# Optimization experiments

Measured on AMD Instinct MI355X. Metric: run time of the kernel, lower is better.

## Reference

```python
import jax, jax.numpy as jnp
import numpy as np
from jax.scipy.stats import norm

N_TOK = 4096
D_MODEL = 1024
D_FF = 2048
N_EXP = 8
K = 2
NOISE_EPS = 0.01          # noise_epsilon in noisy_top_k_gating
LOSS_COEF = 0.1
ZERO_FILL = float(np.finfo(float).eps)  # combined[combined == 0] = eps


def setup_inputs() -> dict:
    key = jax.random.key(0)
    ks = jax.random.split(key, 8)
    s = 0.02
    return {
        "x": jax.random.normal(ks[0], (N_TOK, D_MODEL), jnp.float32),
        "noise": jax.random.normal(ks[1], (N_TOK, N_EXP), jnp.float32),  # torch.randn_like(clean_logits)
        "w_gate": jax.random.normal(ks[2], (D_MODEL, N_EXP), jnp.float32) * s,
        "w_noise": jax.random.normal(ks[3], (D_MODEL, N_EXP), jnp.float32) * s,
        "w1": jax.random.normal(ks[4], (N_EXP, D_MODEL, D_FF), jnp.float32) * s,
        "b1": jnp.zeros((N_EXP, D_FF), jnp.float32),
        "w2": jax.random.normal(ks[5], (N_EXP, D_FF, D_MODEL), jnp.float32) * s,
        "b2": jnp.zeros((N_EXP, D_MODEL), jnp.float32),
    }


def _cv_squared(v):
    # torch .var() is unbiased (ddof=1)
    return jnp.var(v, ddof=1) / (jnp.mean(v) ** 2 + 1e-10)


def reference(x, noise, w_gate, w_noise, w1, b1, w2, b2):
    B = x.shape[0]
    # --- noisy top-k gating (train=True) ---
    clean_logits = x @ w_gate                                   # [B, E]
    noise_stddev = jax.nn.softplus(x @ w_noise) + NOISE_EPS     # [B, E]
    noisy_logits = clean_logits + noise * noise_stddev
    m = min(K + 1, N_EXP)
    top_vals, top_idx = jax.lax.top_k(noisy_logits, m)          # [B, k+1]
    top_k_gates = jax.nn.softmax(top_vals[:, :K], axis=1)       # [B, k]
    gates = jnp.zeros((B, N_EXP), x.dtype).at[
        jnp.arange(B)[:, None], top_idx[:, :K]
    ].set(top_k_gates)                                          # [B, E] sparse-in-values

    # --- load via _prob_in_top_k ---
    thr_in = top_vals[:, K][:, None]       # (k+1)-th noisy value
    thr_out = top_vals[:, K - 1][:, None]  # k-th noisy value
    is_in = noisy_logits > thr_in
    prob_if_in = norm.cdf((clean_logits - thr_in) / noise_stddev)
    prob_if_out = norm.cdf((clean_logits - thr_out) / noise_stddev)
    load = jnp.where(is_in, prob_if_in, prob_if_out).sum(0)     # [E]

    importance = gates.sum(0)
    loss = (_cv_squared(importance) + _cv_squared(load)) * LOSS_COEF

    # --- expert FFNs + gate-weighted combine ---
    # Dense-over-experts evaluation; gates are zero for non-selected experts,
    # so this is mathematically identical to dispatch/combine.
    h = jax.nn.relu(jnp.einsum('td,edf->tef', x, w1) + b1)      # [T, E, d_ff]
    expert_out = jnp.einsum('tef,efd->ted', h, w2) + b2         # [T, E, d_model]
    y = jnp.einsum('ted,te->td', expert_out, gates)             # [T, d_model]
    y = jnp.where(y == 0, ZERO_FILL, y)                         # combined[combined==0] = eps
    return y, loss
```

## Files before the change

### kernel.cpp

```cpp
#include <hip/hip_runtime.h>
#include <hip/hip_bf16.h>

#define N_TOK 4096
#define D_MODEL 1024
#define D_FF 2048
#define N_EXP 8

typedef __attribute__((ext_vector_type(8))) short short8;
typedef __attribute__((ext_vector_type(4))) float f32x4;

#define OFF_COUNTS 0
#define OFF_SEL    128
#define OFF_G0     16512
#define OFF_TOK    32896
#define OFF_GATE   295040
#define OFF_LOADV  426112
#define OFF_XB     1048576
#define OFF_W1T    9437184
#define OFF_W2T    42991616
#define OFF_H      76546048

__device__ __forceinline__ unsigned short f2bf(float f) {
  union { float f; unsigned u; } a; a.f = f;
  return (unsigned short)((a.u + 0x7FFFu + ((a.u >> 16) & 1u)) >> 16);
}

__device__ __forceinline__ void async16(const void* g, void* l) {
  __builtin_amdgcn_global_load_lds(
      (const __attribute__((address_space(1))) unsigned int*)g,
      (__attribute__((address_space(3))) unsigned int*)l, 16, 0, 0);
}

__global__ __launch_bounds__(256) void transpose_both_kernel(
    const float* __restrict__ w1, unsigned short* __restrict__ w1t,
    const float* __restrict__ w2, unsigned short* __restrict__ w2t) {
  const int bx = blockIdx.x;
  const float* in; unsigned short* out;
  int K, N, kb, nb, e;
  if (bx < 4096) {
    K = D_MODEL; N = D_FF;
    e = bx >> 9; const int rem = bx & 511;
    nb = (rem & 31) * 64; kb = (rem >> 5) * 64;
    in = w1; out = w1t;
  } else {
    K = D_FF; N = D_MODEL;
    const int b2x = bx - 4096;
    e = b2x >> 9; const int rem = b2x & 511;
    nb = (rem & 15) * 64; kb = (rem >> 4) * 64;
    in = w2; out = w2t;
  }
  __shared__ float tile[64][65];
  const int tid = threadIdx.x;
  const float* ine = in + (size_t)e * K * N;
  unsigned short* oute = out + (size_t)e * K * N;
  {
    const int c4 = tid & 15, rr = tid >> 4;
#pragma unroll
    for (int i = 0; i < 4; ++i) {
      const int row = i * 16 + rr;
      const float4 v = *(const float4*)(ine + (size_t)(kb + row) * N + nb + c4 * 4);
      tile[row][c4 * 4 + 0] = v.x;
      tile[row][c4 * 4 + 1] = v.y;
      tile[row][c4 * 4 + 2] = v.z;
      tile[row][c4 * 4 + 3] = v.w;
    }
  }
  __syncthreads();
  {
    const int n = tid >> 2, seg = tid & 3;
    unsigned short v[16];
#pragma unroll
    for (int j = 0; j < 16; ++j) v[j] = f2bf(tile[seg * 16 + j][n]);
    uint4* dst = (uint4*)(oute + (size_t)(nb + n) * K + kb + seg * 16);
    dst[0] = *(uint4*)&v[0];
    dst[1] = *(uint4*)&v[8];
  }
}

__global__ __launch_bounds__(256) void gating_kernel(
    const float* __restrict__ x, const float* __restrict__ noise,
    const float* __restrict__ wg, const float* __restrict__ wn,
    int* __restrict__ sel, float* __restrict__ g0out,
    float* __restrict__ loadvec, unsigned short* __restrict__ xb,
    int* __restrict__ counts) {
  if (blockIdx.x == 0 && threadIdx.x < N_EXP) counts[threadIdx.x] = 0;
  const int wave = threadIdx.x >> 6, lane = threadIdx.x & 63;
  const int t = blockIdx.x * 4 + wave;
  float ag[8], an[8];
#pragma unroll
  for (int e = 0; e < 8; ++e) { ag[e] = 0.f; an[e] = 0.f; }
  const float* xrow = x + (size_t)t * D_MODEL;
  for (int d = lane; d < D_MODEL; d += 64) {
    const float xv = xrow[d];
    const float4 wa = ((const float4*)(wg + (size_t)d * 8))[0];
    const float4 wb = ((const float4*)(wg + (size_t)d * 8))[1];
    const float4 na = ((const float4*)(wn + (size_t)d * 8))[0];
    const float4 nb = ((const float4*)(wn + (size_t)d * 8))[1];
    ag[0] += xv * wa.x; ag[1] += xv * wa.y; ag[2] += xv * wa.z; ag[3] += xv * wa.w;
    ag[4] += xv * wb.x; ag[5] += xv * wb.y; ag[6] += xv * wb.z; ag[7] += xv * wb.w;
    an[0] += xv * na.x; an[1] += xv * na.y; an[2] += xv * na.z; an[3] += xv * na.w;
    an[4] += xv * nb.x; an[5] += xv * nb.y; an[6] += xv * nb.z; an[7] += xv * nb.w;
  }
  {
    const float4* xv4 = (const float4*)xrow;
    ushort4* xb4 = (ushort4*)(xb + (size_t)t * D_MODEL);
#pragma unroll
    for (int i = 0; i < 4; ++i) {
      const float4 v = xv4[lane + i * 64];
      ushort4 o;
      o.x = f2bf(v.x); o.y = f2bf(v.y); o.z = f2bf(v.z); o.w = f2bf(v.w);
      xb4[lane + i * 64] = o;
    }
  }
#pragma unroll
  for (int e = 0; e < 8; ++e) {
#pragma unroll
    for (int off = 32; off > 0; off >>= 1) {
      ag[e] += __shfl_xor(ag[e], off, 64);
      an[e] += __shfl_xor(an[e], off, 64);
    }
  }
  float clean[8], sd[8], nz[8];
#pragma unroll
  for (int e = 0; e < 8; ++e) {
    clean[e] = ag[e];
    float s = an[e];
    s = (s > 20.f) ? s : log1pf(expf(s));
    sd[e] = s + 0.01f;
    nz[e] = clean[e] + noise[t * 8 + e] * sd[e];
  }
  float v0 = -1e30f, v1 = -1e30f, v2 = -1e30f; int i0 = 0, i1 = 0;
#pragma unroll
  for (int e = 0; e < 8; ++e) {
    const float v = nz[e];
    if (v > v0)      { v2 = v1; v1 = v0; i1 = i0; v0 = v; i0 = e; }
    else if (v > v1) { v2 = v1; v1 = v; i1 = e; }
    else if (v > v2) { v2 = v; }
  }
  const float ex = expf(v1 - v0);
  const float g0 = 1.f / (1.f + ex);
  if (lane == 0) { sel[t] = i0 | (i1 << 8); g0out[t] = g0; }
  if (lane < 8) {
    const int e = lane;
    const bool is_in = nz[e] > v2;
    const float thr = is_in ? v2 : v1;
    const float z = (clean[e] - thr) / sd[e];
    loadvec[t * 8 + e] = 0.5f * erfcf(-z * 0.70710678118654752f);
  }
}

__global__ __launch_bounds__(256) void build_lists_kernel(
    const int* __restrict__ sel, const float* __restrict__ g0a,
    int* __restrict__ counts, int* __restrict__ tok_list,
    float* __restrict__ gate_list) {
  __shared__ int hist[8], bbase[8];
  if (threadIdx.x < 8) hist[threadIdx.x] = 0;
  __syncthreads();
  const int t = blockIdx.x * 256 + threadIdx.x;
  const int s = sel[t];
  const int e0 = s & 255, e1 = (s >> 8) & 255;
  atomicAdd(&hist[e0], 1);
  atomicAdd(&hist[e1], 1);
  __syncthreads();
  if (threadIdx.x < 8) {
    bbase[threadIdx.x] = atomicAdd(&counts[threadIdx.x], hist[threadIdx.x]);
    hist[threadIdx.x] = 0;
  }
  __syncthreads();
  const float g = g0a[t];
  const int p0 = atomicAdd(&hist[e0], 1);
  const int idx0 = e0 * N_TOK + bbase[e0] + p0;
  tok_list[idx0] = t; gate_list[idx0] = g;
  const int p1 = atomicAdd(&hist[e1], 1);
  const int idx1 = e1 * N_TOK + bbase[e1] + p1;
  tok_list[idx1] = t; gate_list[idx1] = 1.f - g;
}

__global__ __launch_bounds__(256) void gemm1_kernel(
    const unsigned short* __restrict__ xb, const unsigned short* __restrict__ w1t,
    const float* __restrict__ b1,
    const int* __restrict__ counts,
    const int* __restrict__ tok_list, unsigned short* __restrict__ h) {
  const int e = blockIdx.x, nt = blockIdx.y, mt = blockIdx.z;
  const int cnt = counts[e];
  const int m0 = mt * 128;
  if (m0 >= cnt) return;
  int bs = 0;
#pragma unroll
  for (int i = 0; i < 8; ++i) bs += (i < e) ? counts[i] : 0;
  const int n0 = nt * 128;

  __shared__ __align__(16) unsigned short As[128 * 64];
  __shared__ __align__(16) unsigned short Bs[128 * 64];

  const int tid = threadIdx.x;
  const int wave = tid >> 6, lane = tid & 63;
  const int lrow = lane >> 3;
  const int scg  = (lane & 7) ^ lrow;

  const unsigned short* ap[4];
  const unsigned short* bp[4];
  unsigned short* adst[4];
  unsigned short* bdst[4];
#pragma unroll
  for (int c = 0; c < 4; ++c) {
    const int rr = wave * 32 + c * 8;
    const int arow = min(m0 + rr + lrow, cnt - 1);
    const int tok = tok_list[e * N_TOK + arow];
    ap[c] = xb + (size_t)tok * D_MODEL + scg * 8;
    bp[c] = w1t + (size_t)e * D_MODEL * D_FF + (size_t)(n0 + rr + lrow) * D_MODEL + scg * 8;
    adst[c] = As + rr * 64;
    bdst[c] = Bs + rr * 64;
  }

  const int wm = wave & 1, wn = wave >> 1;
  const int q = lane >> 4, r = lane & 15;
  const int r7 = r & 7;

  f32x4 acc[4][4];
#pragma unroll
  for (int a = 0; a < 4; ++a)
#pragma unroll
    for (int b = 0; b < 4; ++b) acc[a][b] = (f32x4){0.f, 0.f, 0.f, 0.f};

  for (int k0 = 0; k0 < D_MODEL; k0 += 64) {
#pragma unroll
    for (int c = 0; c < 4; ++c) {
      async16(ap[c], adst[c]);
      async16(bp[c], bdst[c]);
      ap[c] += 64; bp[c] += 64;
    }
    __syncthreads();
#pragma unroll
    for (int kk = 0; kk < 64; kk += 32) {
      const int gsw = (((kk >> 3) + q) ^ r7) * 8;
      short8 af[4], bfg[4];
#pragma unroll
      for (int t = 0; t < 4; ++t)
        af[t] = *(const short8*)(As + (wm * 64 + t * 16 + r) * 64 + gsw);
#pragma unroll
      for (int t = 0; t < 4; ++t)
        bfg[t] = *(const short8*)(Bs + (wn * 64 + t * 16 + r) * 64 + gsw);
#pragma unroll
      for (int tm = 0; tm < 4; ++tm)
#pragma unroll
        for (int tn = 0; tn < 4; ++tn)
          acc[tm][tn] = __builtin_amdgcn_mfma_f32_16x16x32_bf16(af[tm], bfg[tn], acc[tm][tn], 0, 0, 0);
    }
    __syncthreads();
  }

  float bv[4];
#pragma unroll
  for (int tn = 0; tn < 4; ++tn) bv[tn] = b1[e * D_FF + n0 + wn * 64 + tn * 16 + r];
#pragma unroll
  for (int tm = 0; tm < 4; ++tm) {
#pragma unroll
    for (int v = 0; v < 4; ++v) {
      const int i = wm * 64 + tm * 16 + q * 4 + v;
      if (m0 + i < cnt) {
        unsigned short* hrow = h + (size_t)(bs + m0 + i) * D_FF + n0 + wn * 64 + r;
#pragma unroll
        for (int tn = 0; tn < 4; ++tn)
          hrow[tn * 16] = f2bf(fmaxf(acc[tm][tn][v] + bv[tn], 0.f));
      }
    }
  }
}

__global__ __launch_bounds__(256) void gemm2_kernel(
    const unsigned short* __restrict__ h, const unsigned short* __restrict__ w2t,
    const float* __restrict__ b2,
    const int* __restrict__ counts,
    const int* __restrict__ tok_list, const float* __restrict__ gate_list,
    float* __restrict__ y) {
  const int e = blockIdx.x, nt = blockIdx.y;
  const int mt = blockIdx.z >> 1, kh = blockIdx.z & 1;
  const int cnt = counts[e];
  const int m0 = mt * 128;
  if (m0 >= cnt) return;
  int bs = 0;
#pragma unroll
  for (int i = 0; i < 8; ++i) bs += (i < e) ? counts[i] : 0;
  const int n0 = nt * 128;
  const int kbase = kh * (D_FF / 2);

  __shared__ __align__(16) unsigned short As[128 * 64];
  __shared__ __align__(16) unsigned short Bs[128 * 64];

  const int tid = threadIdx.x;
  const int wave = tid >> 6, lane = tid & 63;
  const int lrow = lane >> 3;
  const int scg  = (lane & 7) ^ lrow;

  const unsigned short* ap[4];
  const unsigned short* bp[4];
  unsigned short* adst[4];
  unsigned short* bdst[4];
#pragma unroll
  for (int c = 0; c < 4; ++c) {
    const int rr = wave * 32 + c * 8;
    const int arow = min(m0 + rr + lrow, cnt - 1);
    ap[c] = h + (size_t)(bs + arow) * D_FF + kbase + scg * 8;
    bp[c] = w2t + (size_t)e * D_MODEL * D_FF + (size_t)(n0 + rr + lrow) * D_FF + kbase + scg * 8;
    adst[c] = As + rr * 64;
    bdst[c] = Bs + rr * 64;
  }

  const int wm = wave & 1, wn = wave >> 1;
  const int q = lane >> 4, r = lane & 15;
  const int r7 = r & 7;

  f32x4 acc[4][4];
#pragma unroll
  for (int a = 0; a < 4; ++a)
#pragma unroll
    for (int b = 0; b < 4; ++b) acc[a][b] = (f32x4){0.f, 0.f, 0.f, 0.f};

  for (int k0 = 0; k0 < D_FF / 2; k0 += 64) {
#pragma unroll
    for (int c = 0; c < 4; ++c) {
      async16(ap[c], adst[c]);
      async16(bp[c], bdst[c]);
      ap[c] += 64; bp[c] += 64;
    }
    __syncthreads();
#pragma unroll
    for (int kk = 0; kk < 64; kk += 32) {
      const int gsw = (((kk >> 3) + q) ^ r7) * 8;
      short8 af[4], bfg[4];
#pragma unroll
      for (int t = 0; t < 4; ++t)
        af[t] = *(const short8*)(As + (wm * 64 + t * 16 + r) * 64 + gsw);
#pragma unroll
      for (int t = 0; t < 4; ++t)
        bfg[t] = *(const short8*)(Bs + (wn * 64 + t * 16 + r) * 64 + gsw);
#pragma unroll
      for (int tm = 0; tm < 4; ++tm)
#pragma unroll
        for (int tn = 0; tn < 4; ++tn)
          acc[tm][tn] = __builtin_amdgcn_mfma_f32_16x16x32_bf16(af[tm], bfg[tn], acc[tm][tn], 0, 0, 0);
    }
    __syncthreads();
  }

  float bv[4];
#pragma unroll
  for (int tn = 0; tn < 4; ++tn)
    bv[tn] = (kh == 0) ? b2[e * D_MODEL + n0 + wn * 64 + tn * 16 + r] : 0.f;
#pragma unroll
  for (int tm = 0; tm < 4; ++tm) {
#pragma unroll
    for (int v = 0; v < 4; ++v) {
      const int i = wm * 64 + tm * 16 + q * 4 + v;
      const int mrow = m0 + i;
      if (mrow < cnt) {
        const int idx = e * N_TOK + mrow;
        const int tok = tok_list[idx];
        const float g = gate_list[idx];
        float* orow = y + (size_t)tok * D_MODEL + n0 + wn * 64 + r;
#pragma unroll
        for (int tn = 0; tn < 4; ++tn)
          atomicAdd(&orow[tn * 16], (acc[tm][tn][v] + bv[tn]) * g);
      }
    }
  }
}

__global__ __launch_bounds__(256) void fixup_loss_kernel(
    float* __restrict__ y,
    const int* __restrict__ sel, const float* __restrict__ g0a,
    const float* __restrict__ loadvec) {
  const int i = blockIdx.x * 256 + threadIdx.x;
  float4 o = ((const float4*)y)[i];
  const float eps = 2.2204460492503131e-16f;
  if (o.x == 0.f) o.x = eps;
  if (o.y == 0.f) o.y = eps;
  if (o.z == 0.f) o.z = eps;
  if (o.w == 0.f) o.w = eps;
  ((float4*)y)[i] = o;

  if (blockIdx.x == 0) {
    float limp[8], lld[8];
#pragma unroll
    for (int e = 0; e < 8; ++e) { limp[e] = 0.f; lld[e] = 0.f; }
    for (int t = threadIdx.x; t < N_TOK; t += 256) {
      const int s = sel[t];
      const float g = g0a[t];
      const int e0 = s & 255, e1 = (s >> 8) & 255;
#pragma unroll
      for (int e = 0; e < 8; ++e)
        limp[e] += (e0 == e ? g : 0.f) + (e1 == e ? (1.f - g) : 0.f);
#pragma unroll
      for (int e = 0; e < 8; ++e) lld[e] += loadvec[t * 8 + e];
    }
#pragma unroll
    for (int e = 0; e < 8; ++e) {
#pragma unroll
      for (int off = 32; off > 0; off >>= 1) {
        limp[e] += __shfl_xor(limp[e], off, 64);
        lld[e]  += __shfl_xor(lld[e],  off, 64);
      }
    }
    __shared__ float red[4][16];
    const int wave = threadIdx.x >> 6, lane = threadIdx.x & 63;
    if (lane == 0) {
#pragma unroll
      for (int e = 0; e < 8; ++e) { red[wave][e] = limp[e]; red[wave][8 + e] = lld[e]; }
    }
    __syncthreads();
    if (threadIdx.x == 0) {
      double imp[8], ld[8];
      for (int e = 0; e < 8; ++e) {
        imp[e] = (double)red[0][e] + red[1][e] + red[2][e] + red[3][e];
        ld[e]  = (double)red[0][8 + e] + red[1][8 + e] + red[2][8 + e] + red[3][8 + e];
      }
      double mi = 0, ml = 0;
      for (int e = 0; e < 8; ++e) { mi += imp[e]; ml += ld[e]; }
      mi /= 8.0; ml /= 8.0;
      double vi = 0, vl = 0;
      for (int e = 0; e < 8; ++e) { vi += (imp[e] - mi) * (imp[e] - mi); vl += (ld[e] - ml) * (ld[e] - ml); }
      vi /= 7.0; vl /= 7.0;
      y[(size_t)N_TOK * D_MODEL] =
          (float)(0.1 * (vi / (mi * mi + 1e-10) + vl / (ml * ml + 1e-10)));
    }
  }
}

extern "C" void kernel_launch(void* const* d_in, const int* in_sizes, int n_in,
                              void* d_out, int out_size, void* d_ws, size_t ws_size,
                              hipStream_t stream) {
  const float* x     = (const float*)d_in[0];
  const float* noise = (const float*)d_in[1];
  const float* wg    = (const float*)d_in[2];
  const float* wn    = (const float*)d_in[3];
  const float* w1    = (const float*)d_in[4];
  const float* b1    = (const float*)d_in[5];
  const float* w2    = (const float*)d_in[6];
  const float* b2    = (const float*)d_in[7];
  float* out = (float*)d_out;

  char* ws = (char*)d_ws;
  int*   counts    = (int*)(ws + OFF_COUNTS);
  int*   sel       = (int*)(ws + OFF_SEL);
  float* g0a       = (float*)(ws + OFF_G0);
  int*   tok_list  = (int*)(ws + OFF_TOK);
  float* gate_list = (float*)(ws + OFF_GATE);
  float* loadvec   = (float*)(ws + OFF_LOADV);
  unsigned short* xb  = (unsigned short*)(ws + OFF_XB);
  unsigned short* w1t = (unsigned short*)(ws + OFF_W1T);
  unsigned short* w2t = (unsigned short*)(ws + OFF_W2T);
  unsigned short* h   = (unsigned short*)(ws + OFF_H);

  hipMemsetAsync(out, 0, (size_t)N_TOK * D_MODEL * sizeof(float), stream);

  gating_kernel<<<N_TOK / 4, 256, 0, stream>>>(x, noise, wg, wn, sel, g0a, loadvec, xb, counts);
  transpose_both_kernel<<<8192, 256, 0, stream>>>(w1, w1t, w2, w2t);
  build_lists_kernel<<<N_TOK / 256, 256, 0, stream>>>(sel, g0a, counts, tok_list, gate_list);
  gemm1_kernel<<<dim3(N_EXP, D_FF / 128, N_TOK / 128), 256, 0, stream>>>(
      xb, w1t, b1, counts, tok_list, h);
  gemm2_kernel<<<dim3(N_EXP, D_MODEL / 128, (N_TOK / 128) * 2), 256, 0, stream>>>(
      h, w2t, b2, counts, tok_list, gate_list, out);
  fixup_loss_kernel<<<(N_TOK * D_MODEL / 4) / 256, 256, 0, stream>>>(out, sel, g0a, loadvec);
}
```

Before: 383.3 us.

## Fuse MoE pipeline into one cooperative persistent kernel with split-output buffers

Merges the gating, weight transpose, list building, both expert GEMMs and the final fixup into a single cooperative persistent kernel, with grid.sync between phases. The second GEMM stops using atomicAdd into a zeroed output and instead writes into per-slot, per-K-half staging buffers that a final pass sums, so the output memset is gone as well. This removes several launches and the atomic contention, but adds grid-wide barriers, limits occupancy to what a cooperative launch allows, and adds extra staging traffic. The sout1 buffer reuses the w1t region after GEMM1 has finished with it.

```diff
diff --git a/kernel.cpp b/kernel.cpp
--- a/kernel.cpp
+++ b/kernel.cpp
@@ -1,5 +1,8 @@
 #include <hip/hip_runtime.h>
 #include <hip/hip_bf16.h>
+#include <hip/hip_cooperative_groups.h>
+
+namespace cg = cooperative_groups;
 
 #define N_TOK 4096
 #define D_MODEL 1024
@@ -19,6 +22,7 @@
 #define OFF_W1T    9437184
 #define OFF_W2T    42991616
 #define OFF_H      76546048
+#define OFF_SOUT   110100480
 
 __device__ __forceinline__ unsigned short f2bf(float f) {
   union { float f; unsigned u; } a; a.f = f;
@@ -31,398 +35,403 @@
       (__attribute__((address_space(3))) unsigned int*)l, 16, 0, 0);
 }
 
-__global__ __launch_bounds__(256) void transpose_both_kernel(
-    const float* __restrict__ w1, unsigned short* __restrict__ w1t,
-    const float* __restrict__ w2, unsigned short* __restrict__ w2t) {
-  const int bx = blockIdx.x;
-  const float* in; unsigned short* out;
-  int K, N, kb, nb, e;
-  if (bx < 4096) {
-    K = D_MODEL; N = D_FF;
-    e = bx >> 9; const int rem = bx & 511;
-    nb = (rem & 31) * 64; kb = (rem >> 5) * 64;
-    in = w1; out = w1t;
-  } else {
-    K = D_FF; N = D_MODEL;
-    const int b2x = bx - 4096;
-    e = b2x >> 9; const int rem = b2x & 511;
-    nb = (rem & 15) * 64; kb = (rem >> 4) * 64;
-    in = w2; out = w2t;
-  }
-  __shared__ float tile[64][65];
-  const int tid = threadIdx.x;
-  const float* ine = in + (size_t)e * K * N;
-  unsigned short* oute = out + (size_t)e * K * N;
-  {
-    const int c4 = tid & 15, rr = tid >> 4;
-#pragma unroll
-    for (int i = 0; i < 4; ++i) {
-      const int row = i * 16 + rr;
-      const float4 v = *(const float4*)(ine + (size_t)(kb + row) * N + nb + c4 * 4);
-      tile[row][c4 * 4 + 0] = v.x;
-      tile[row][c4 * 4 + 1] = v.y;
-      tile[row][c4 * 4 + 2] = v.z;
-      tile[row][c4 * 4 + 3] = v.w;
-    }
-  }
-  __syncthreads();
-  {
-    const int n = tid >> 2, seg = tid & 3;
-    unsigned short v[16];
-#pragma unroll
-    for (int j = 0; j < 16; ++j) v[j] = f2bf(tile[seg * 16 + j][n]);
-    uint4* dst = (uint4*)(oute + (size_t)(nb + n) * K + kb + seg * 16);
-    dst[0] = *(uint4*)&v[0];
-    dst[1] = *(uint4*)&v[8];
-  }
-}
-
-__global__ __launch_bounds__(256) void gating_kernel(
+__global__ __launch_bounds__(256, 3) void moe_mega_kernel(
     const float* __restrict__ x, const float* __restrict__ noise,
     const float* __restrict__ wg, const float* __restrict__ wn,
-    int* __restrict__ sel, float* __restrict__ g0out,
+    const float* __restrict__ w1, const float* __restrict__ b1,
+    const float* __restrict__ w2, const float* __restrict__ b2,
+    float* __restrict__ y,
+    int* __restrict__ sel, float* __restrict__ g0a,
+    int* __restrict__ tok_list, float* __restrict__ gate_list,
     float* __restrict__ loadvec, unsigned short* __restrict__ xb,
+    unsigned short* __restrict__ w1t, unsigned short* __restrict__ w2t,
+    unsigned short* __restrict__ h,
+    float* __restrict__ sout0, float* __restrict__ sout1,
     int* __restrict__ counts) {
-  if (blockIdx.x == 0 && threadIdx.x < N_EXP) counts[threadIdx.x] = 0;
-  const int wave = threadIdx.x >> 6, lane = threadIdx.x & 63;
-  const int t = blockIdx.x * 4 + wave;
-  float ag[8], an[8];
-#pragma unroll
-  for (int e = 0; e < 8; ++e) { ag[e] = 0.f; an[e] = 0.f; }
-  const float* xrow = x + (size_t)t * D_MODEL;
-  for (int d = lane; d < D_MODEL; d += 64) {
-    const float xv = xrow[d];
-    const float4 wa = ((const float4*)(wg + (size_t)d * 8))[0];
-    const float4 wb = ((const float4*)(wg + (size_t)d * 8))[1];
-    const float4 na = ((const float4*)(wn + (size_t)d * 8))[0];
-    const float4 nb = ((const float4*)(wn + (size_t)d * 8))[1];
-    ag[0] += xv * wa.x; ag[1] += xv * wa.y; ag[2] += xv * wa.z; ag[3] += xv * wa.w;
-    ag[4] += xv * wb.x; ag[5] += xv * wb.y; ag[6] += xv * wb.z; ag[7] += xv * wb.w;
-    an[0] += xv * na.x; an[1] += xv * na.y; an[2] += xv * na.z; an[3] += xv * na.w;
-    an[4] += xv * nb.x; an[5] += xv * nb.y; an[6] += xv * nb.z; an[7] += xv * nb.w;
+  __shared__ __align__(16) unsigned char smem[32768];
+  cg::grid_group grid = cg::this_grid();
+  const int b = blockIdx.x, tid = threadIdx.x;
+  const int nblk = gridDim.x;
+  const int wave = tid >> 6, lane = tid & 63;
+
+  if (b == 0 && tid < N_EXP) counts[tid] = 0;
+#pragma unroll 1
+  for (int t = b * 4 + wave; t < N_TOK; t += nblk * 4) {
+    float ag[8], an[8];
+#pragma unroll
+    for (int e = 0; e < 8; ++e) { ag[e] = 0.f; an[e] = 0.f; }
+    const float* xrow = x + (size_t)t * D_MODEL;
+    for (int d = lane; d < D_MODEL; d += 64) {
+      const float xv = xrow[d];
+      const float4 wa = ((const float4*)(wg + (size_t)d * 8))[0];
+      const float4 wb = ((const float4*)(wg + (size_t)d * 8))[1];
+      const float4 na = ((const float4*)(wn + (size_t)d * 8))[0];
+      const float4 nb = ((const float4*)(wn + (size_t)d * 8))[1];
+      ag[0] += xv * wa.x; ag[1] += xv * wa.y; ag[2] += xv * wa.z; ag[3] += xv * wa.w;
+      ag[4] += xv * wb.x; ag[5] += xv * wb.y; ag[6] += xv * wb.z; ag[7] += xv * wb.w;
+      an[0] += xv * na.x; an[1] += xv * na.y; an[2] += xv * na.z; an[3] += xv * na.w;
+      an[4] += xv * nb.x; an[5] += xv * nb.y; an[6] += xv * nb.z; an[7] += xv * nb.w;
+    }
+    {
+      const float4* xv4 = (const float4*)xrow;
+      ushort4* xb4 = (ushort4*)(xb + (size_t)t * D_MODEL);
+#pragma unroll
+      for (int i = 0; i < 4; ++i) {
+        const float4 v = xv4[lane + i * 64];
+        ushort4 o;
+        o.x = f2bf(v.x); o.y = f2bf(v.y); o.z = f2bf(v.z); o.w = f2bf(v.w);
+        xb4[lane + i * 64] = o;
+      }
+    }
+#pragma unroll
+    for (int e = 0; e < 8; ++e) {
+#pragma unroll
+      for (int off = 32; off > 0; off >>= 1) {
+        ag[e] += __shfl_xor(ag[e], off, 64);
+        an[e] += __shfl_xor(an[e], off, 64);
+      }
+    }
+    float clean[8], sd[8], nz[8];
+#pragma unroll
+    for (int e = 0; e < 8; ++e) {
+      clean[e] = ag[e];
+      float s = an[e];
+      s = (s > 20.f) ? s : log1pf(expf(s));
+      sd[e] = s + 0.01f;
+      nz[e] = clean[e] + noise[t * 8 + e] * sd[e];
+    }
+    float v0 = -1e30f, v1 = -1e30f, v2 = -1e30f; int i0 = 0, i1 = 0;
+#pragma unroll
+    for (int e = 0; e < 8; ++e) {
+      const float v = nz[e];
+      if (v > v0)      { v2 = v1; v1 = v0; i1 = i0; v0 = v; i0 = e; }
+      else if (v > v1) { v2 = v1; v1 = v; i1 = e; }
+      else if (v > v2) { v2 = v; }
+    }
+    const float ex = expf(v1 - v0);
+    const float g0 = 1.f / (1.f + ex);
+    if (lane == 0) { sel[t] = i0 | (i1 << 8); g0a[t] = g0; }
+    if (lane < 8) {
+      const int e = lane;
+      const bool is_in = nz[e] > v2;
+      const float thr = is_in ? v2 : v1;
+      const float z = (clean[e] - thr) / sd[e];
+      loadvec[t * 8 + e] = 0.5f * erfcf(-z * 0.70710678118654752f);
+    }
   }
   {
-    const float4* xv4 = (const float4*)xrow;
-    ushort4* xb4 = (ushort4*)(xb + (size_t)t * D_MODEL);
-#pragma unroll
-    for (int i = 0; i < 4; ++i) {
-      const float4 v = xv4[lane + i * 64];
-      ushort4 o;
-      o.x = f2bf(v.x); o.y = f2bf(v.y); o.z = f2bf(v.z); o.w = f2bf(v.w);
-      xb4[lane + i * 64] = o;
-    }
-  }
-#pragma unroll
-  for (int e = 0; e < 8; ++e) {
-#pragma unroll
-    for (int off = 32; off > 0; off >>= 1) {
-      ag[e] += __shfl_xor(ag[e], off, 64);
-      an[e] += __shfl_xor(an[e], off, 64);
-    }
-  }
-  float clean[8], sd[8], nz[8];
-#pragma unroll
-  for (int e = 0; e < 8; ++e) {
-    clean[e] = ag[e];
-    float s = an[e];
-    s = (s > 20.f) ? s : log1pf(expf(s));
-    sd[e] = s + 0.01f;
-    nz[e] = clean[e] + noise[t * 8 + e] * sd[e];
-  }
-  float v0 = -1e30f, v1 = -1e30f, v2 = -1e30f; int i0 = 0, i1 = 0;
-#pragma unroll
-  for (int e = 0; e < 8; ++e) {
-    const float v = nz[e];
-    if (v > v0)      { v2 = v1; v1 = v0; i1 = i0; v0 = v; i0 = e; }
-    else if (v > v1) { v2 = v1; v1 = v; i1 = e; }
-    else if (v > v2) { v2 = v; }
-  }
-  const float ex = expf(v1 - v0);
-  const float g0 = 1.f / (1.f + ex);
-  if (lane == 0) { sel[t] = i0 | (i1 << 8); g0out[t] = g0; }
-  if (lane < 8) {
-    const int e = lane;
-    const bool is_in = nz[e] > v2;
-    const float thr = is_in ? v2 : v1;
-    const float z = (clean[e] - thr) / sd[e];
-    loadvec[t * 8 + e] = 0.5f * erfcf(-z * 0.70710678118654752f);
-  }
-}
-
-__global__ __launch_bounds__(256) void build_lists_kernel(
-    const int* __restrict__ sel, const float* __restrict__ g0a,
-    int* __restrict__ counts, int* __restrict__ tok_list,
-    float* __restrict__ gate_list) {
-  __shared__ int hist[8], bbase[8];
-  if (threadIdx.x < 8) hist[threadIdx.x] = 0;
-  __syncthreads();
-  const int t = blockIdx.x * 256 + threadIdx.x;
-  const int s = sel[t];
-  const int e0 = s & 255, e1 = (s >> 8) & 255;
-  atomicAdd(&hist[e0], 1);
-  atomicAdd(&hist[e1], 1);
-  __syncthreads();
-  if (threadIdx.x < 8) {
-    bbase[threadIdx.x] = atomicAdd(&counts[threadIdx.x], hist[threadIdx.x]);
-    hist[threadIdx.x] = 0;
-  }
-  __syncthreads();
-  const float g = g0a[t];
-  const int p0 = atomicAdd(&hist[e0], 1);
-  const int idx0 = e0 * N_TOK + bbase[e0] + p0;
-  tok_list[idx0] = t; gate_list[idx0] = g;
-  const int p1 = atomicAdd(&hist[e1], 1);
-  const int idx1 = e1 * N_TOK + bbase[e1] + p1;
-  tok_list[idx1] = t; gate_list[idx1] = 1.f - g;
-}
-
-__global__ __launch_bounds__(256) void gemm1_kernel(
-    const unsigned short* __restrict__ xb, const unsigned short* __restrict__ w1t,
-    const float* __restrict__ b1,
-    const int* __restrict__ counts,
-    const int* __restrict__ tok_list, unsigned short* __restrict__ h) {
-  const int e = blockIdx.x, nt = blockIdx.y, mt = blockIdx.z;
-  const int cnt = counts[e];
-  const int m0 = mt * 128;
-  if (m0 >= cnt) return;
-  int bs = 0;
-#pragma unroll
-  for (int i = 0; i < 8; ++i) bs += (i < e) ? counts[i] : 0;
-  const int n0 = nt * 128;
-
-  __shared__ __align__(16) unsigned short As[128 * 64];
-  __shared__ __align__(16) unsigned short Bs[128 * 64];
-
-  const int tid = threadIdx.x;
-  const int wave = tid >> 6, lane = tid & 63;
-  const int lrow = lane >> 3;
-  const int scg  = (lane & 7) ^ lrow;
-
-  const unsigned short* ap[4];
-  const unsigned short* bp[4];
-  unsigned short* adst[4];
-  unsigned short* bdst[4];
-#pragma unroll
-  for (int c = 0; c < 4; ++c) {
-    const int rr = wave * 32 + c * 8;
-    const int arow = min(m0 + rr + lrow, cnt - 1);
-    const int tok = tok_list[e * N_TOK + arow];
-    ap[c] = xb + (size_t)tok * D_MODEL + scg * 8;
-    bp[c] = w1t + (size_t)e * D_MODEL * D_FF + (size_t)(n0 + rr + lrow) * D_MODEL + scg * 8;
-    adst[c] = As + rr * 64;
-    bdst[c] = Bs + rr * 64;
-  }
-
-  const int wm = wave & 1, wn = wave >> 1;
-  const int q = lane >> 4, r = lane & 15;
-  const int r7 = r & 7;
-
-  f32x4 acc[4][4];
-#pragma unroll
-  for (int a = 0; a < 4; ++a)
-#pragma unroll
-    for (int b = 0; b < 4; ++b) acc[a][b] = (f32x4){0.f, 0.f, 0.f, 0.f};
-
-  for (int k0 = 0; k0 < D_MODEL; k0 += 64) {
-#pragma unroll
-    for (int c = 0; c < 4; ++c) {
-      async16(ap[c], adst[c]);
-      async16(bp[c], bdst[c]);
-      ap[c] += 64; bp[c] += 64;
-    }
+    float (*tile)[65] = (float(*)[65])smem;
+#pragma unroll 1
+    for (int bx = b; bx < 8192; bx += nblk) {
+      const float* in; unsigned short* out;
+      int K, N, kb, nb, e;
+      if (bx < 4096) {
+        K = D_MODEL; N = D_FF;
+        e = bx >> 9; const int rem = bx & 511;
+        nb = (rem & 31) * 64; kb = (rem >> 5) * 64;
+        in = w1; out = w1t;
+      } else {
+        K = D_FF; N = D_MODEL;
+        const int b2x = bx - 4096;
+        e = b2x >> 9; const int rem = b2x & 511;
+        nb = (rem & 15) * 64; kb = (rem >> 4) * 64;
+        in = w2; out = w2t;
+      }
+      const float* ine = in + (size_t)e * K * N;
+      unsigned short* oute = out + (size_t)e * K * N;
+      {
+        const int c4 = tid & 15, rr = tid >> 4;
+#pragma unroll
+        for (int j = 0; j < 4; ++j) {
+          const int row = j * 16 + rr;
+          const float4 v = *(const float4*)(ine + (size_t)(kb + row) * N + nb + c4 * 4);
+          tile[row][c4 * 4 + 0] = v.x;
+          tile[row][c4 * 4 + 1] = v.y;
+          tile[row][c4 * 4 + 2] = v.z;
+          tile[row][c4 * 4 + 3] = v.w;
+        }
+      }
+      __syncthreads();
+      {
+        const int n = tid >> 2, seg = tid & 3;
+        unsigned short v[16];
+#pragma unroll
+        for (int j = 0; j < 16; ++j) v[j] = f2bf(tile[seg * 16 + j][n]);
+        uint4* dst = (uint4*)(oute + (size_t)(nb + n) * K + kb + seg * 16);
+        dst[0] = *(uint4*)&v[0];
+        dst[1] = *(uint4*)&v[8];
+      }
+      __syncthreads();
+    }
+  }
+
+  grid.sync();
+  if (b < 16) {
+    int* hist = (int*)smem;
+    int* bbase = hist + 8;
+    if (tid < 8) hist[tid] = 0;
     __syncthreads();
-#pragma unroll
-    for (int kk = 0; kk < 64; kk += 32) {
-      const int gsw = (((kk >> 3) + q) ^ r7) * 8;
-      short8 af[4], bfg[4];
-#pragma unroll
-      for (int t = 0; t < 4; ++t)
-        af[t] = *(const short8*)(As + (wm * 64 + t * 16 + r) * 64 + gsw);
-#pragma unroll
-      for (int t = 0; t < 4; ++t)
-        bfg[t] = *(const short8*)(Bs + (wn * 64 + t * 16 + r) * 64 + gsw);
-#pragma unroll
-      for (int tm = 0; tm < 4; ++tm)
-#pragma unroll
-        for (int tn = 0; tn < 4; ++tn)
-          acc[tm][tn] = __builtin_amdgcn_mfma_f32_16x16x32_bf16(af[tm], bfg[tn], acc[tm][tn], 0, 0, 0);
-    }
+    const int t = b * 256 + tid;
+    const int s = sel[t];
+    const int e0 = s & 255, e1 = (s >> 8) & 255;
+    atomicAdd(&hist[e0], 1);
+    atomicAdd(&hist[e1], 1);
     __syncthreads();
-  }
-
-  float bv[4];
-#pragma unroll
-  for (int tn = 0; tn < 4; ++tn) bv[tn] = b1[e * D_FF + n0 + wn * 64 + tn * 16 + r];
-#pragma unroll
-  for (int tm = 0; tm < 4; ++tm) {
-#pragma unroll
-    for (int v = 0; v < 4; ++v) {
-      const int i = wm * 64 + tm * 16 + q * 4 + v;
-      if (m0 + i < cnt) {
-        unsigned short* hrow = h + (size_t)(bs + m0 + i) * D_FF + n0 + wn * 64 + r;
-#pragma unroll
-        for (int tn = 0; tn < 4; ++tn)
-          hrow[tn * 16] = f2bf(fmaxf(acc[tm][tn][v] + bv[tn], 0.f));
-      }
-    }
-  }
-}
-
-__global__ __launch_bounds__(256) void gemm2_kernel(
-    const unsigned short* __restrict__ h, const unsigned short* __restrict__ w2t,
-    const float* __restrict__ b2,
-    const int* __restrict__ counts,
-    const int* __restrict__ tok_list, const float* __restrict__ gate_list,
-    float* __restrict__ y) {
-  const int e = blockIdx.x, nt = blockIdx.y;
-  const int mt = blockIdx.z >> 1, kh = blockIdx.z & 1;
-  const int cnt = counts[e];
-  const int m0 = mt * 128;
-  if (m0 >= cnt) return;
-  int bs = 0;
-#pragma unroll
-  for (int i = 0; i < 8; ++i) bs += (i < e) ? counts[i] : 0;
-  const int n0 = nt * 128;
-  const int kbase = kh * (D_FF / 2);
-
-  __shared__ __align__(16) unsigned short As[128 * 64];
-  __shared__ __align__(16) unsigned short Bs[128 * 64];
-
-  const int tid = threadIdx.x;
-  const int wave = tid >> 6, lane = tid & 63;
-  const int lrow = lane >> 3;
-  const int scg  = (lane & 7) ^ lrow;
-
-  const unsigned short* ap[4];
-  const unsigned short* bp[4];
-  unsigned short* adst[4];
-  unsigned short* bdst[4];
-#pragma unroll
-  for (int c = 0; c < 4; ++c) {
-    const int rr = wave * 32 + c * 8;
-    const int arow = min(m0 + rr + lrow, cnt - 1);
-    ap[c] = h + (size_t)(bs + arow) * D_FF + kbase + scg * 8;
-    bp[c] = w2t + (size_t)e * D_MODEL * D_FF + (size_t)(n0 + rr + lrow) * D_FF + kbase + scg * 8;
-    adst[c] = As + rr * 64;
-    bdst[c] = Bs + rr * 64;
-  }
-
-  const int wm = wave & 1, wn = wave >> 1;
-  const int q = lane >> 4, r = lane & 15;
-  const int r7 = r & 7;
-
-  f32x4 acc[4][4];
-#pragma unroll
-  for (int a = 0; a < 4; ++a)
-#pragma unroll
-    for (int b = 0; b < 4; ++b) acc[a][b] = (f32x4){0.f, 0.f, 0.f, 0.f};
-
-  for (int k0 = 0; k0 < D_FF / 2; k0 += 64) {
-#pragma unroll
-    for (int c = 0; c < 4; ++c) {
-      async16(ap[c], adst[c]);
-      async16(bp[c], bdst[c]);
-      ap[c] += 64; bp[c] += 64;
+    if (tid < 8) {
+      bbase[tid] = atomicAdd(&counts[tid], hist[tid]);
+      hist[tid] = 0;
     }
     __syncthreads();
-#pragma unroll
-    for (int kk = 0; kk < 64; kk += 32) {
-      const int gsw = (((kk >> 3) + q) ^ r7) * 8;
-      short8 af[4], bfg[4];
-#pragma unroll
-      for (int t = 0; t < 4; ++t)
-        af[t] = *(const short8*)(As + (wm * 64 + t * 16 + r) * 64 + gsw);
-#pragma unroll
-      for (int t = 0; t < 4; ++t)
-        bfg[t] = *(const short8*)(Bs + (wn * 64 + t * 16 + r) * 64 + gsw);
-#pragma unroll
-      for (int tm = 0; tm < 4; ++tm)
-#pragma unroll
-        for (int tn = 0; tn < 4; ++tn)
-          acc[tm][tn] = __builtin_amdgcn_mfma_f32_16x16x32_bf16(af[tm], bfg[tn], acc[tm][tn], 0, 0, 0);
-    }
-    __syncthreads();
-  }
-
-  float bv[4];
-#pragma unroll
-  for (int tn = 0; tn < 4; ++tn)
-    bv[tn] = (kh == 0) ? b2[e * D_MODEL + n0 + wn * 64 + tn * 16 + r] : 0.f;
-#pragma unroll
-  for (int tm = 0; tm < 4; ++tm) {
-#pragma unroll
-    for (int v = 0; v < 4; ++v) {
-      const int i = wm * 64 + tm * 16 + q * 4 + v;
-      const int mrow = m0 + i;
-      if (mrow < cnt) {
-        const int idx = e * N_TOK + mrow;
-        const int tok = tok_list[idx];
-        const float g = gate_list[idx];
-        float* orow = y + (size_t)tok * D_MODEL + n0 + wn * 64 + r;
-#pragma unroll
-        for (int tn = 0; tn < 4; ++tn)
-          atomicAdd(&orow[tn * 16], (acc[tm][tn][v] + bv[tn]) * g);
-      }
-    }
-  }
-}
-
-__global__ __launch_bounds__(256) void fixup_loss_kernel(
-    float* __restrict__ y,
-    const int* __restrict__ sel, const float* __restrict__ g0a,
-    const float* __restrict__ loadvec) {
-  const int i = blockIdx.x * 256 + threadIdx.x;
-  float4 o = ((const float4*)y)[i];
-  const float eps = 2.2204460492503131e-16f;
-  if (o.x == 0.f) o.x = eps;
-  if (o.y == 0.f) o.y = eps;
-  if (o.z == 0.f) o.z = eps;
-  if (o.w == 0.f) o.w = eps;
-  ((float4*)y)[i] = o;
-
-  if (blockIdx.x == 0) {
-    float limp[8], lld[8];
-#pragma unroll
-    for (int e = 0; e < 8; ++e) { limp[e] = 0.f; lld[e] = 0.f; }
-    for (int t = threadIdx.x; t < N_TOK; t += 256) {
-      const int s = sel[t];
-      const float g = g0a[t];
-      const int e0 = s & 255, e1 = (s >> 8) & 255;
-#pragma unroll
-      for (int e = 0; e < 8; ++e)
-        limp[e] += (e0 == e ? g : 0.f) + (e1 == e ? (1.f - g) : 0.f);
-#pragma unroll
-      for (int e = 0; e < 8; ++e) lld[e] += loadvec[t * 8 + e];
-    }
-#pragma unroll
-    for (int e = 0; e < 8; ++e) {
-#pragma unroll
-      for (int off = 32; off > 0; off >>= 1) {
-        limp[e] += __shfl_xor(limp[e], off, 64);
-        lld[e]  += __shfl_xor(lld[e],  off, 64);
-      }
-    }
-    __shared__ float red[4][16];
-    const int wave = threadIdx.x >> 6, lane = threadIdx.x & 63;
-    if (lane == 0) {
-#pragma unroll
-      for (int e = 0; e < 8; ++e) { red[wave][e] = limp[e]; red[wave][8 + e] = lld[e]; }
-    }
-    __syncthreads();
-    if (threadIdx.x == 0) {
-      double imp[8], ld[8];
+    const float g = g0a[t];
+    const int p0 = atomicAdd(&hist[e0], 1);
+    const int idx0 = e0 * N_TOK + bbase[e0] + p0;
+    tok_list[idx0] = t; gate_list[idx0] = g;
+    const int p1 = atomicAdd(&hist[e1], 1);
+    const int idx1 = e1 * N_TOK + bbase[e1] + p1;
+    tok_list[idx1] = t | (1 << 16); gate_list[idx1] = 1.f - g;
+  }
+
+  grid.sync();
+  {
+    unsigned short* As = (unsigned short*)smem;
+    unsigned short* Bs = As + 128 * 64;
+    const int lrow = lane >> 3;
+    const int scg  = (lane & 7) ^ lrow;
+    const int wm = wave & 1, wn2 = wave >> 1;
+    const int q = lane >> 4, r = lane & 15;
+    const int r7 = r & 7;
+#pragma unroll 1
+    for (int jj = b; jj < 4096; jj += nblk) {
+      const int e = jj & 7, nt = (jj >> 3) & 15, mt = jj >> 7;
+      const int cnt = counts[e];
+      const int m0 = mt * 128;
+      if (m0 >= cnt) continue;
+      int bs = 0;
+#pragma unroll
+      for (int i = 0; i < 8; ++i) bs += (i < e) ? counts[i] : 0;
+      const int n0 = nt * 128;
+
+      const unsigned short* ap[4];
+      const unsigned short* bp[4];
+      unsigned short* adst[4];
+      unsigned short* bdst[4];
+#pragma unroll
+      for (int c = 0; c < 4; ++c) {
+        const int rr = wave * 32 + c * 8;
+        const int arow = min(m0 + rr + lrow, cnt - 1);
+        const int tok = tok_list[e * N_TOK + arow] & 0xFFFF;
+        ap[c] = xb + (size_t)tok * D_MODEL + scg * 8;
+        bp[c] = w1t + (size_t)e * D_MODEL * D_FF + (size_t)(n0 + rr + lrow) * D_MODEL + scg * 8;
+        adst[c] = As + rr * 64;
+        bdst[c] = Bs + rr * 64;
+      }
+      f32x4 acc[4][4];
+#pragma unroll
+      for (int a = 0; a < 4; ++a)
+#pragma unroll
+        for (int c = 0; c < 4; ++c) acc[a][c] = (f32x4){0.f, 0.f, 0.f, 0.f};
+
+      for (int k0 = 0; k0 < D_MODEL; k0 += 64) {
+#pragma unroll
+        for (int c = 0; c < 4; ++c) {
+          async16(ap[c], adst[c]);
+          async16(bp[c], bdst[c]);
+          ap[c] += 64; bp[c] += 64;
+        }
+        __syncthreads();
+#pragma unroll
+        for (int kk = 0; kk < 64; kk += 32) {
+          const int gsw = (((kk >> 3) + q) ^ r7) * 8;
+          short8 af[4], bfg[4];
+#pragma unroll
+          for (int t = 0; t < 4; ++t)
+            af[t] = *(const short8*)(As + (wm * 64 + t * 16 + r) * 64 + gsw);
+#pragma unroll
+          for (int t = 0; t < 4; ++t)
+            bfg[t] = *(const short8*)(Bs + (wn2 * 64 + t * 16 + r) * 64 + gsw);
+#pragma unroll
+          for (int tm = 0; tm < 4; ++tm)
+#pragma unroll
+            for (int tn = 0; tn < 4; ++tn)
+              acc[tm][tn] = __builtin_amdgcn_mfma_f32_16x16x32_bf16(af[tm], bfg[tn], acc[tm][tn], 0, 0, 0);
+        }
+        __syncthreads();
+      }
+      float bv[4];
+#pragma unroll
+      for (int tn = 0; tn < 4; ++tn) bv[tn] = b1[e * D_FF + n0 + wn2 * 64 + tn * 16 + r];
+#pragma unroll
+      for (int tm = 0; tm < 4; ++tm) {
+#pragma unroll
+        for (int v = 0; v < 4; ++v) {
+          const int i = wm * 64 + tm * 16 + q * 4 + v;
+          if (m0 + i < cnt) {
+            unsigned short* hrow = h + (size_t)(bs + m0 + i) * D_FF + n0 + wn2 * 64 + r;
+#pragma unroll
+            for (int tn = 0; tn < 4; ++tn)
+              hrow[tn * 16] = f2bf(fmaxf(acc[tm][tn][v] + bv[tn], 0.f));
+          }
+        }
+      }
+    }
+  }
+
+  grid.sync();
+  {
+    unsigned short* As = (unsigned short*)smem;
+    unsigned short* Bs = As + 128 * 64;
+    const int lrow = lane >> 3;
+    const int scg  = (lane & 7) ^ lrow;
+    const int wm = wave & 1, wn2 = wave >> 1;
+    const int q = lane >> 4, r = lane & 15;
+    const int r7 = r & 7;
+#pragma unroll 1
+    for (int jj = b; jj < 4096; jj += nblk) {
+      const int e = jj & 7, nt = (jj >> 3) & 7;
+      const int kh = (jj >> 6) & 1, mt = jj >> 7;
+      const int cnt = counts[e];
+      const int m0 = mt * 128;
+      if (m0 >= cnt) continue;
+      int bs = 0;
+#pragma unroll
+      for (int i = 0; i < 8; ++i) bs += (i < e) ? counts[i] : 0;
+      const int n0 = nt * 128;
+      const int kbase = kh * (D_FF / 2);
+
+      const unsigned short* ap[4];
+      const unsigned short* bp[4];
+      unsigned short* adst[4];
+      unsigned short* bdst[4];
+#pragma unroll
+      for (int c = 0; c < 4; ++c) {
+        const int rr = wave * 32 + c * 8;
+        const int arow = min(m0 + rr + lrow, cnt - 1);
+        ap[c] = h + (size_t)(bs + arow) * D_FF + kbase + scg * 8;
+        bp[c] = w2t + (size_t)e * D_MODEL * D_FF + (size_t)(n0 + rr + lrow) * D_FF + kbase + scg * 8;
+        adst[c] = As + rr * 64;
+        bdst[c] = Bs + rr * 64;
+      }
+      f32x4 acc[4][4];
+#pragma unroll
+      for (int a = 0; a < 4; ++a)
+#pragma unroll
+        for (int c = 0; c < 4; ++c) acc[a][c] = (f32x4){0.f, 0.f, 0.f, 0.f};
+
+      for (int k0 = 0; k0 < D_FF / 2; k0 += 64) {
+#pragma unroll
+        for (int c = 0; c < 4; ++c) {
+          async16(ap[c], adst[c]);
+          async16(bp[c], bdst[c]);
+          ap[c] += 64; bp[c] += 64;
+        }
+        __syncthreads();
+#pragma unroll
+        for (int kk = 0; kk < 64; kk += 32) {
+          const int gsw = (((kk >> 3) + q) ^ r7) * 8;
+          short8 af[4], bfg[4];
+#pragma unroll
+          for (int t = 0; t < 4; ++t)
+            af[t] = *(const short8*)(As + (wm * 64 + t * 16 + r) * 64 + gsw);
+#pragma unroll
+          for (int t = 0; t < 4; ++t)
+            bfg[t] = *(const short8*)(Bs + (wn2 * 64 + t * 16 + r) * 64 + gsw);
+#pragma unroll
+          for (int tm = 0; tm < 4; ++tm)
+#pragma unroll
+            for (int tn = 0; tn < 4; ++tn)
+              acc[tm][tn] = __builtin_amdgcn_mfma_f32_16x16x32_bf16(af[tm], bfg[tn], acc[tm][tn], 0, 0, 0);
+        }
+        __syncthreads();
+      }
+      float bv[4];
+#pragma unroll
+      for (int tn = 0; tn < 4; ++tn)
+        bv[tn] = (kh == 0) ? b2[e * D_MODEL + n0 + wn2 * 64 + tn * 16 + r] : 0.f;
+      float* const souts = (kh == 0) ? sout0 : sout1;
+#pragma unroll
+      for (int tm = 0; tm < 4; ++tm) {
+#pragma unroll
+        for (int v = 0; v < 4; ++v) {
+          const int i = wm * 64 + tm * 16 + q * 4 + v;
+          const int mrow = m0 + i;
+          if (mrow < cnt) {
+            const int pv = tok_list[e * N_TOK + mrow];
+            const int tok = pv & 0xFFFF, sl = pv >> 16;
+            const float g = gate_list[e * N_TOK + mrow];
+            float* orow = souts + ((size_t)sl * N_TOK + tok) * D_MODEL + n0 + wn2 * 64 + r;
+#pragma unroll
+            for (int tn = 0; tn < 4; ++tn)
+              orow[tn * 16] = (acc[tm][tn][v] + bv[tn]) * g;
+          }
+        }
+      }
+    }
+  }
+
+  grid.sync();
+  {
+#pragma unroll 1
+    for (int idx = b * 256 + tid; idx < N_TOK * D_MODEL / 4; idx += nblk * 256) {
+      const float4 a = ((const float4*)sout0)[idx];
+      const float4 c = ((const float4*)sout1)[idx];
+      const float4 bb = ((const float4*)(sout0 + (size_t)N_TOK * D_MODEL))[idx];
+      const float4 d = ((const float4*)(sout1 + (size_t)N_TOK * D_MODEL))[idx];
+      float4 o;
+      o.x = (a.x + c.x) + (bb.x + d.x);
+      o.y = (a.y + c.y) + (bb.y + d.y);
+      o.z = (a.z + c.z) + (bb.z + d.z);
+      o.w = (a.w + c.w) + (bb.w + d.w);
+      const float eps = 2.2204460492503131e-16f;
+      if (o.x == 0.f) o.x = eps;
+      if (o.y == 0.f) o.y = eps;
+      if (o.z == 0.f) o.z = eps;
+      if (o.w == 0.f) o.w = eps;
+      ((float4*)y)[idx] = o;
+    }
+    if (b == 0) {
+      float limp[8], lld[8];
+#pragma unroll
+      for (int e = 0; e < 8; ++e) { limp[e] = 0.f; lld[e] = 0.f; }
+      for (int t = tid; t < N_TOK; t += 256) {
+        const int s = sel[t];
+        const float g = g0a[t];
+        const int e0 = s & 255, e1 = (s >> 8) & 255;
+#pragma unroll
+        for (int e = 0; e < 8; ++e)
+          limp[e] += (e0 == e ? g : 0.f) + (e1 == e ? (1.f - g) : 0.f);
+#pragma unroll
+        for (int e = 0; e < 8; ++e) lld[e] += loadvec[t * 8 + e];
+      }
+#pragma unroll
       for (int e = 0; e < 8; ++e) {
-        imp[e] = (double)red[0][e] + red[1][e] + red[2][e] + red[3][e];
-        ld[e]  = (double)red[0][8 + e] + red[1][8 + e] + red[2][8 + e] + red[3][8 + e];
-      }
-      double mi = 0, ml = 0;
-      for (int e = 0; e < 8; ++e) { mi += imp[e]; ml += ld[e]; }
-      mi /= 8.0; ml /= 8.0;
-      double vi = 0, vl = 0;
-      for (int e = 0; e < 8; ++e) { vi += (imp[e] - mi) * (imp[e] - mi); vl += (ld[e] - ml) * (ld[e] - ml); }
-      vi /= 7.0; vl /= 7.0;
-      y[(size_t)N_TOK * D_MODEL] =
-          (float)(0.1 * (vi / (mi * mi + 1e-10) + vl / (ml * ml + 1e-10)));
+#pragma unroll
+        for (int off = 32; off > 0; off >>= 1) {
+          limp[e] += __shfl_xor(limp[e], off, 64);
+          lld[e]  += __shfl_xor(lld[e],  off, 64);
+        }
+      }
+      float* redf = (float*)smem;
+      __syncthreads();
+      if (lane == 0) {
+#pragma unroll
+        for (int e = 0; e < 8; ++e) { redf[wave * 16 + e] = limp[e]; redf[wave * 16 + 8 + e] = lld[e]; }
+      }
+      __syncthreads();
+      if (tid == 0) {
+        double imp[8], ld[8];
+        for (int e = 0; e < 8; ++e) {
+          imp[e] = (double)redf[e] + redf[16 + e] + redf[32 + e] + redf[48 + e];
+          ld[e]  = (double)redf[8 + e] + redf[24 + e] + redf[40 + e] + redf[56 + e];
+        }
+        double mi = 0, ml = 0;
+        for (int e = 0; e < 8; ++e) { mi += imp[e]; ml += ld[e]; }
+        mi /= 8.0; ml /= 8.0;
+        double vi = 0, vl = 0;
+        for (int e = 0; e < 8; ++e) { vi += (imp[e] - mi) * (imp[e] - mi); vl += (ld[e] - ml) * (ld[e] - ml); }
+        vi /= 7.0; vl /= 7.0;
+        y[(size_t)N_TOK * D_MODEL] =
+            (float)(0.1 * (vi / (mi * mi + 1e-10) + vl / (ml * ml + 1e-10)));
+      }
     }
   }
 }
@@ -451,15 +460,24 @@
   unsigned short* w1t = (unsigned short*)(ws + OFF_W1T);
   unsigned short* w2t = (unsigned short*)(ws + OFF_W2T);
   unsigned short* h   = (unsigned short*)(ws + OFF_H);
-
-  hipMemsetAsync(out, 0, (size_t)N_TOK * D_MODEL * sizeof(float), stream);
-
-  gating_kernel<<<N_TOK / 4, 256, 0, stream>>>(x, noise, wg, wn, sel, g0a, loadvec, xb, counts);
-  transpose_both_kernel<<<8192, 256, 0, stream>>>(w1, w1t, w2, w2t);
-  build_lists_kernel<<<N_TOK / 256, 256, 0, stream>>>(sel, g0a, counts, tok_list, gate_list);
-  gemm1_kernel<<<dim3(N_EXP, D_FF / 128, N_TOK / 128), 256, 0, stream>>>(
-      xb, w1t, b1, counts, tok_list, h);
-  gemm2_kernel<<<dim3(N_EXP, D_MODEL / 128, (N_TOK / 128) * 2), 256, 0, stream>>>(
-      h, w2t, b2, counts, tok_list, gate_list, out);
-  fixup_loss_kernel<<<(N_TOK * D_MODEL / 4) / 256, 256, 0, stream>>>(out, sel, g0a, loadvec);
+  float* sout0 = (float*)(ws + OFF_SOUT);
+  float* sout1 = (float*)(ws + OFF_W1T);
+
+  int maxb = 0;
+  hipOccupancyMaxActiveBlocksPerMultiprocessor(&maxb, moe_mega_kernel, 256, 0);
+  if (maxb <= 0) maxb = 3;
+  int nblk = maxb * 256;
+  if (nblk > 1024) nblk = 1024;
+  if (nblk < 16) nblk = 16;
+
+  void* args[] = {
+    (void*)&x, (void*)&noise, (void*)&wg, (void*)&wn,
+    (void*)&w1, (void*)&b1, (void*)&w2, (void*)&b2,
+    (void*)&out,
+    (void*)&sel, (void*)&g0a, (void*)&tok_list, (void*)&gate_list,
+    (void*)&loadvec, (void*)&xb, (void*)&w1t, (void*)&w2t, (void*)&h,
+    (void*)&sout0, (void*)&sout1, (void*)&counts,
+  };
+  hipLaunchCooperativeKernel((void*)moe_mega_kernel, dim3(nblk), dim3(256),
+                             args, 0, stream);
 }
```

Result: slower. 560.3 us (+46.2%).
